# Kernel tuning notes

Measured on AMD Instinct MI355X. Metric: run time of the kernel, lower is better.

Reference implementation:

```python
import jax, jax.numpy as jnp
import numpy as np

B, N, F, R, DEG, STEPS = 4, 1024, 128, 16, 16, 2


def setup_inputs() -> dict:
    key = jax.random.key(0)
    ks = jax.random.split(key, 12)
    BN = B * N
    E = BN * DEG

    def edges(k):
        # edges kept within each graph of size N, then offset per graph
        e = jax.random.randint(k, (2, E), 0, N)
        off = jnp.repeat(jnp.arange(B, dtype=jnp.int32) * N, N * DEG)
        return e + off[None, :]

    return {
        "x_s": jax.random.normal(ks[0], (BN, F), jnp.float32),
        "edge_index_s": edges(ks[1]),
        "x_t": jax.random.normal(ks[2], (BN, F), jnp.float32),
        "edge_index_t": edges(ks[3]),
        "W1_self": jax.random.normal(ks[4], (F, F), jnp.float32) / np.float32(np.sqrt(F)),
        "W1_nbr": jax.random.normal(ks[5], (F, F), jnp.float32) / np.float32(np.sqrt(F)),
        "b1": jnp.zeros((F,), jnp.float32),
        "W2_self": jax.random.normal(ks[6], (R, R), jnp.float32) / np.float32(np.sqrt(R)),
        "W2_nbr": jax.random.normal(ks[7], (R, R), jnp.float32) / np.float32(np.sqrt(R)),
        "b2": jnp.zeros((R,), jnp.float32),
        "Wm1": jax.random.normal(ks[8], (R, R), jnp.float32) / np.float32(np.sqrt(R)),
        "bm1": jnp.zeros((R,), jnp.float32),
        "Wm2": jax.random.normal(ks[9], (R, 1), jnp.float32) / np.float32(np.sqrt(R)),
        "bm2": jnp.zeros((1,), jnp.float32),
        "r_steps": jax.random.normal(ks[10], (STEPS, B, N, R), jnp.float32),
    }


def _psi(x, ei, Ws, Wn, b):
    # simple GraphConv: self transform + summed neighbor transform
    agg = jax.ops.segment_sum(x[ei[0]], ei[1], num_segments=x.shape[0])
    return jax.nn.relu(x @ Ws + agg @ Wn + b)


def reference(x_s, edge_index_s, x_t, edge_index_t, W1_self, W1_nbr, b1,
              W2_self, W2_nbr, b2, Wm1, bm1, Wm2, bm2, r_steps):
    # psi_1 on both graphs, then dense-batch to [B, N, F] (equal-size graphs,
    # so masks are all-True and masked_softmax == softmax)
    h_s = _psi(x_s, edge_index_s, W1_self, W1_nbr, b1).reshape(B, N, F)
    h_t = _psi(x_t, edge_index_t, W1_self, W1_nbr, b1).reshape(B, N, F)

    S_hat = jnp.einsum('bsf,btf->bst', h_s, h_t)  # [B, Ns, Nt]
    S_0 = jax.nn.softmax(S_hat, axis=-1)

    for i in range(STEPS):
        S = jax.nn.softmax(S_hat, axis=-1)
        r_s = r_steps[i]                             # [B, N, R]
        r_t = jnp.einsum('bst,bsr->btr', S, r_s)     # S^T @ r_s
        o_s = _psi(r_s.reshape(B * N, R), edge_index_s, W2_self, W2_nbr, b2).reshape(B, N, R)
        o_t = _psi(r_t.reshape(B * N, R), edge_index_t, W2_self, W2_nbr, b2).reshape(B, N, R)
        D = o_s[:, :, None, :] - o_t[:, None, :, :]  # [B, Ns, Nt, R]
        upd = (jax.nn.relu(D @ Wm1 + bm1) @ Wm2 + bm2)[..., 0]
        S_hat = S_hat + upd

    S_L = jax.nn.softmax(S_hat, axis=-1)
    return (S_0, S_L)
```

## Files before the change

kernel.cpp:

```cpp
#include <hip/hip_runtime.h>

#define B_ 4
#define N_ 1024
#define F_ 128
#define R_ 16
#define E_ 65536
#define BN_ 4096

__global__ __launch_bounds__(256) void hist_k(
    const int* __restrict__ eis, const int* __restrict__ eit, int* __restrict__ counts) {
  const int* ei = blockIdx.y ? eit : eis;
  int* c = counts + blockIdx.y * BN_;
  int e = blockIdx.x * 256 + threadIdx.x;
  atomicAdd(c + ei[E_ + e], 1);
}

__global__ __launch_bounds__(256) void csr_scan(
    const int* __restrict__ counts, int* __restrict__ offs, int* __restrict__ cursor) {
  const int* c = counts + blockIdx.x * BN_;
  int* o = offs + blockIdx.x * (BN_ + 1);
  int* cur = cursor + blockIdx.x * BN_;
  int tid = threadIdx.x;
  int base = tid * 16;
  int local[16], sum = 0;
#pragma unroll
  for (int i = 0; i < 16; i++) { local[i] = sum; sum += c[base + i]; }
  __shared__ int csum[256];
  csum[tid] = sum;
  __syncthreads();
  for (int d = 1; d < 256; d <<= 1) {
    int v = (tid >= d) ? csum[tid - d] : 0;
    __syncthreads();
    csum[tid] += v;
    __syncthreads();
  }
  int prev = (tid == 0) ? 0 : csum[tid - 1];
#pragma unroll
  for (int i = 0; i < 16; i++) { int off = prev + local[i]; o[base + i] = off; cur[base + i] = off; }
  if (tid == 255) o[BN_] = csum[255];
}

__global__ __launch_bounds__(256) void csr_fill(
    const int* __restrict__ eis, const int* __restrict__ eit,
    int* __restrict__ cursor, int* __restrict__ csr) {
  const int* ei = blockIdx.y ? eit : eis;
  int* cur = cursor + blockIdx.y * BN_;
  int* cs = csr + blockIdx.y * E_;
  int e = blockIdx.x * 256 + threadIdx.x;
  int src = ei[e], dst = ei[E_ + e];
  int pos = atomicAdd(cur + dst, 1);
  cs[pos] = src;
}

__global__ __launch_bounds__(256) void gather_f(
    const float* __restrict__ xs, const float* __restrict__ xt,
    const int* __restrict__ csr, const int* __restrict__ offs,
    float* __restrict__ aggs, float* __restrict__ aggt) {
  const float* x = blockIdx.y ? xt : xs;
  const int* cs = csr + blockIdx.y * E_;
  const int* of = offs + blockIdx.y * (BN_ + 1);
  float* agg = blockIdx.y ? aggt : aggs;
  int node = blockIdx.x * 8 + (threadIdx.x >> 5);
  int ch4 = (threadIdx.x & 31) * 4;
  int j0 = of[node], j1 = of[node + 1];
  float4 a0 = {0, 0, 0, 0}, a1 = {0, 0, 0, 0}, a2 = {0, 0, 0, 0}, a3 = {0, 0, 0, 0};
  int j = j0;
  for (; j + 3 < j1; j += 4) {
    int s0 = cs[j], s1 = cs[j + 1], s2 = cs[j + 2], s3 = cs[j + 3];
    float4 v0 = *(const float4*)(x + (size_t)s0 * F_ + ch4);
    float4 v1 = *(const float4*)(x + (size_t)s1 * F_ + ch4);
    float4 v2 = *(const float4*)(x + (size_t)s2 * F_ + ch4);
    float4 v3 = *(const float4*)(x + (size_t)s3 * F_ + ch4);
    a0.x += v0.x; a0.y += v0.y; a0.z += v0.z; a0.w += v0.w;
    a1.x += v1.x; a1.y += v1.y; a1.z += v1.z; a1.w += v1.w;
    a2.x += v2.x; a2.y += v2.y; a2.z += v2.z; a2.w += v2.w;
    a3.x += v3.x; a3.y += v3.y; a3.z += v3.z; a3.w += v3.w;
  }
  for (; j < j1; j++) {
    float4 v = *(const float4*)(x + (size_t)cs[j] * F_ + ch4);
    a0.x += v.x; a0.y += v.y; a0.z += v.z; a0.w += v.w;
  }
  float4 o;
  o.x = (a0.x + a1.x) + (a2.x + a3.x);
  o.y = (a0.y + a1.y) + (a2.y + a3.y);
  o.z = (a0.z + a1.z) + (a2.z + a3.z);
  o.w = (a0.w + a1.w) + (a2.w + a3.w);
  *(float4*)(agg + (size_t)node * F_ + ch4) = o;
}

__global__ __launch_bounds__(256) void psi1_gemm(
    const float* __restrict__ xs, const float* __restrict__ aggs,
    const float* __restrict__ xt, const float* __restrict__ aggt,
    const float* __restrict__ Ws, const float* __restrict__ Wn,
    const float* __restrict__ bias, float* __restrict__ hs, float* __restrict__ ht) {
  const float* x   = blockIdx.z ? xt   : xs;
  const float* agg = blockIdx.z ? aggt : aggs;
  float*       h   = blockIdx.z ? ht   : hs;
  int n0 = blockIdx.x * 64, m0 = blockIdx.y * 64;
  int tid = threadIdx.x, tx = tid & 15, ty = tid >> 4;
  __shared__ __align__(16) float sA[16][68];
  __shared__ __align__(16) float sB[16][68];
  float acc[4][4] = {};
  for (int phase = 0; phase < 2; phase++) {
    const float* A  = phase ? agg : x;
    const float* Bw = phase ? Wn  : Ws;
    for (int kb = 0; kb < F_; kb += 16) {
      int row = tid >> 2, k4 = (tid & 3) * 4;
      float4 va = *(const float4*)(A + (size_t)(m0 + row) * F_ + kb + k4);
      sA[k4 + 0][row] = va.x; sA[k4 + 1][row] = va.y;
      sA[k4 + 2][row] = va.z; sA[k4 + 3][row] = va.w;
      int k = tid >> 4, n4 = (tid & 15) * 4;
      *(float4*)&sB[k][n4] = *(const float4*)(Bw + (size_t)(kb + k) * F_ + n0 + n4);
      __syncthreads();
#pragma unroll
      for (int kk = 0; kk < 16; kk++) {
        float a[4], bb[4];
        *(float4*)a  = *(const float4*)&sA[kk][ty * 4];
        *(float4*)bb = *(const float4*)&sB[kk][tx * 4];
#pragma unroll
        for (int i = 0; i < 4; i++)
#pragma unroll
          for (int j = 0; j < 4; j++) acc[i][j] += a[i] * bb[j];
      }
      __syncthreads();
    }
  }
  float4 bv = *(const float4*)(bias + n0 + tx * 4);
  float bj[4] = {bv.x, bv.y, bv.z, bv.w};
#pragma unroll
  for (int i = 0; i < 4; i++) {
    int m = m0 + ty * 4 + i;
    float4 o;
    o.x = fmaxf(acc[i][0] + bj[0], 0.f); o.y = fmaxf(acc[i][1] + bj[1], 0.f);
    o.z = fmaxf(acc[i][2] + bj[2], 0.f); o.w = fmaxf(acc[i][3] + bj[3], 0.f);
    *(float4*)(h + (size_t)m * F_ + n0 + tx * 4) = o;
  }
}

__global__ __launch_bounds__(256) void shat_gemm(
    const float* __restrict__ hs, const float* __restrict__ ht, float* __restrict__ S) {
  int b = blockIdx.z;
  int n0 = blockIdx.x * 128, m0 = blockIdx.y * 128;
  int tid = threadIdx.x, tx = tid & 15, ty = tid >> 4;
  __shared__ __align__(16) float sA[16][132];
  __shared__ __align__(16) float sB[16][132];
  float acc[8][8] = {};
  const float* Ag = hs + (size_t)(b * N_ + m0) * F_;
  const float* Bg = ht + (size_t)(b * N_ + n0) * F_;
  for (int kb = 0; kb < F_; kb += 16) {
#pragma unroll
    for (int l = 0; l < 2; l++) {
      int idx = tid + l * 256;
      int row = idx >> 2, k4 = (idx & 3) * 4;
      float4 va = *(const float4*)(Ag + (size_t)row * F_ + kb + k4);
      sA[k4 + 0][row] = va.x; sA[k4 + 1][row] = va.y;
      sA[k4 + 2][row] = va.z; sA[k4 + 3][row] = va.w;
      float4 vb = *(const float4*)(Bg + (size_t)row * F_ + kb + k4);
      sB[k4 + 0][row] = vb.x; sB[k4 + 1][row] = vb.y;
      sB[k4 + 2][row] = vb.z; sB[k4 + 3][row] = vb.w;
    }
    __syncthreads();
#pragma unroll
    for (int kk = 0; kk < 16; kk++) {
      float a[8], bb[8];
      *(float4*)&a[0]  = *(const float4*)&sA[kk][ty * 8];
      *(float4*)&a[4]  = *(const float4*)&sA[kk][ty * 8 + 4];
      *(float4*)&bb[0] = *(const float4*)&sB[kk][tx * 8];
      *(float4*)&bb[4] = *(const float4*)&sB[kk][tx * 8 + 4];
#pragma unroll
      for (int i = 0; i < 8; i++)
#pragma unroll
        for (int j = 0; j < 8; j++) acc[i][j] += a[i] * bb[j];
    }
    __syncthreads();
  }
#pragma unroll
  for (int i = 0; i < 8; i++) {
    size_t off = ((size_t)(b * N_ + m0 + ty * 8 + i)) * N_ + n0 + tx * 8;
    float4 o0 = {acc[i][0], acc[i][1], acc[i][2], acc[i][3]};
    float4 o1 = {acc[i][4], acc[i][5], acc[i][6], acc[i][7]};
    *(float4*)(S + off) = o0; *(float4*)(S + off + 4) = o1;
  }
}

__global__ __launch_bounds__(256) void row_stats(
    const float* __restrict__ in, float2* __restrict__ stats) {
  int row = blockIdx.x;
  float4 v = ((const float4*)(in + (size_t)row * N_))[threadIdx.x];
  float m = fmaxf(fmaxf(v.x, v.y), fmaxf(v.z, v.w));
#pragma unroll
  for (int o = 32; o > 0; o >>= 1) m = fmaxf(m, __shfl_down(m, o, 64));
  __shared__ float rmax[4], rsum[4];
  int wave = threadIdx.x >> 6, lane = threadIdx.x & 63;
  if (lane == 0) rmax[wave] = m;
  __syncthreads();
  m = fmaxf(fmaxf(rmax[0], rmax[1]), fmaxf(rmax[2], rmax[3]));
  float s = __expf(v.x - m) + __expf(v.y - m) + __expf(v.z - m) + __expf(v.w - m);
#pragma unroll
  for (int o = 32; o > 0; o >>= 1) s += __shfl_down(s, o, 64);
  if (lane == 0) rsum[wave] = s;
  __syncthreads();
  if (threadIdx.x == 0) {
    float tot = rsum[0] + rsum[1] + rsum[2] + rsum[3];
    stats[row] = make_float2(m, 1.f / tot);
  }
}

template <bool WRITE_S>
__global__ __launch_bounds__(256) void rt_part_k(
    const float* __restrict__ S, const float2* __restrict__ stats,
    const float* __restrict__ rs, float* __restrict__ part, float* __restrict__ Sout) {
  int b = blockIdx.z, c = blockIdx.y, t0 = blockIdx.x * 256;
  int tid = threadIdx.x;
  int s0 = c * 32;
  __shared__ float rsh[32][16];
  __shared__ float sstat[64];
  if (tid < 128) {
    int srow = tid >> 2, c4 = (tid & 3) * 4;
    float4 v = *(const float4*)(rs + ((size_t)(b * N_ + s0 + srow)) * R_ + c4);
    rsh[srow][c4] = v.x; rsh[srow][c4 + 1] = v.y;
    rsh[srow][c4 + 2] = v.z; rsh[srow][c4 + 3] = v.w;
  } else if (tid < 192) {
    sstat[tid - 128] = ((const float*)(stats + b * N_ + s0))[tid - 128];
  }
  __syncthreads();
  float acc[16] = {};
  const size_t base = ((size_t)(b * N_ + s0)) * N_ + t0 + tid;
  const float* Sp = S + base;
  float* So = WRITE_S ? (Sout + base) : nullptr;
#pragma unroll
  for (int s = 0; s < 32; s++) {
    float p = __expf(Sp[(size_t)s * N_] - sstat[2 * s]) * sstat[2 * s + 1];
    if (WRITE_S) So[(size_t)s * N_] = p;
#pragma unroll
    for (int r = 0; r < 16; r++) acc[r] += p * rsh[s][r];
  }
  float* o = part + ((size_t)((b * 32 + c) * N_) + t0 + tid) * R_;
  *(float4*)(o + 0)  = *(float4*)&acc[0];
  *(float4*)(o + 4)  = *(float4*)&acc[4];
  *(float4*)(o + 8)  = *(float4*)&acc[8];
  *(float4*)(o + 12) = *(float4*)&acc[12];
}

__global__ __launch_bounds__(256) void rt_reduce(
    const float* __restrict__ part, float* __restrict__ rt) {
  int gid = blockIdx.x * 256 + threadIdx.x;
  int b = gid >> 12, tr = gid & 4095;
  const float* p = part + (size_t)b * (32 * N_ * R_) + (size_t)tr * 4;
  float4 acc = {0.f, 0.f, 0.f, 0.f};
#pragma unroll
  for (int c = 0; c < 32; c++) {
    float4 v = *(const float4*)(p + (size_t)c * (N_ * R_));
    acc.x += v.x; acc.y += v.y; acc.z += v.z; acc.w += v.w;
  }
  ((float4*)rt)[gid] = acc;
}

__global__ __launch_bounds__(256) void gpsi2p(
    const float* __restrict__ vs, const float* __restrict__ vt,
    const int* __restrict__ csr, const int* __restrict__ offs,
    const float* __restrict__ W2s, const float* __restrict__ W2n,
    const float* __restrict__ b2, const float* __restrict__ Wm1,
    float* __restrict__ Ps, float* __restrict__ Pt4) {
  const float* v = blockIdx.y ? vt : vs;
  const int* cs = csr + blockIdx.y * E_;
  const int* of = offs + blockIdx.y * (BN_ + 1);
  int col = threadIdx.x & 15, row = threadIdx.x >> 4;
  int node = blockIdx.x * 16 + row;
  int j0 = of[node], j1 = of[node + 1];
  float a0 = 0.f, a1 = 0.f, a2 = 0.f, a3 = 0.f;
  int j = j0;
  for (; j + 3 < j1; j += 4) {
    int s0 = cs[j], s1 = cs[j + 1], s2 = cs[j + 2], s3 = cs[j + 3];
    a0 += v[(size_t)s0 * R_ + col];
    a1 += v[(size_t)s1 * R_ + col];
    a2 += v[(size_t)s2 * R_ + col];
    a3 += v[(size_t)s3 * R_ + col];
  }
  for (; j < j1; j++) a0 += v[(size_t)cs[j] * R_ + col];
  __shared__ float sWs[16][16], sWn[16][16], sWm[16][17];
  __shared__ float sv[16][17], sa[16][17], so[16][17];
  sWs[row][col] = W2s[row * 16 + col];
  sWn[row][col] = W2n[row * 16 + col];
  sWm[row][col] = Wm1[row * 16 + col];
  sv[row][col] = v[(size_t)node * R_ + col];
  sa[row][col] = (a0 + a1) + (a2 + a3);
  __syncthreads();
  float o = b2[col];
#pragma unroll
  for (int k = 0; k < 16; k++) o += sv[row][k] * sWs[k][col] + sa[row][k] * sWn[k][col];
  so[row][col] = fmaxf(o, 0.f);
  __syncthreads();
  float p = 0;
#pragma unroll
  for (int k = 0; k < 16; k++) p += so[row][k] * sWm[k][col];
  if (blockIdx.y) {
    Pt4[((size_t)(col >> 2) * BN_ + node) * 4 + (col & 3)] = p;
  } else {
    Ps[(size_t)node * R_ + col] = p;
  }
}

template <int LAST>
__global__ __launch_bounds__(256) void upd_row4(
    float* __restrict__ Shat, const float* __restrict__ Ps, const float* __restrict__ Pt4,
    const float* __restrict__ bm1, const float* __restrict__ Wm2,
    const float* __restrict__ bm2, float2* __restrict__ stats, float* __restrict__ SL) {
  int b = blockIdx.y, s0 = blockIdx.x * 2;
  int tid = threadIdx.x;
  __shared__ float sc[2][16], sw16[16];
  __shared__ float wred[2][4];
  if (tid < 32) sc[tid >> 4][tid & 15] =
      Ps[((size_t)(b * N_ + s0 + (tid >> 4))) * R_ + (tid & 15)] + bm1[tid & 15];
  if (tid < 16) sw16[tid] = Wm2[tid];
  float bm2v = bm2[0];
  __syncthreads();
  float vals[2][4];
#pragma unroll
  for (int tile = 0; tile < 4; tile++) {
    int gt = b * N_ + tile * 256 + tid;
    float pt[16];
    *(float4*)&pt[0]  = *(const float4*)(Pt4 + ((size_t)0 * BN_ + gt) * 4);
    *(float4*)&pt[4]  = *(const float4*)(Pt4 + ((size_t)1 * BN_ + gt) * 4);
    *(float4*)&pt[8]  = *(const float4*)(Pt4 + ((size_t)2 * BN_ + gt) * 4);
    *(float4*)&pt[12] = *(const float4*)(Pt4 + ((size_t)3 * BN_ + gt) * 4);
#pragma unroll
    for (int rr = 0; rr < 2; rr++) {
      size_t off = ((size_t)(b * N_ + s0 + rr)) * N_ + tile * 256 + tid;
      float sum = bm2v;
#pragma unroll
      for (int r = 0; r < 16; r++) sum += fmaxf(sc[rr][r] - pt[r], 0.f) * sw16[r];
      float vv = Shat[off] + sum;
      vals[rr][tile] = vv;
      if (!LAST) Shat[off] = vv;
    }
  }
  int wave = tid >> 6, lane = tid & 63;
#pragma unroll
  for (int rr = 0; rr < 2; rr++) {
    float m = fmaxf(fmaxf(vals[rr][0], vals[rr][1]), fmaxf(vals[rr][2], vals[rr][3]));
#pragma unroll
    for (int o = 32; o > 0; o >>= 1) m = fmaxf(m, __shfl_down(m, o, 64));
    if (lane == 0) wred[rr][wave] = m;
  }
  __syncthreads();
  float M[2];
#pragma unroll
  for (int rr = 0; rr < 2; rr++)
    M[rr] = fmaxf(fmaxf(wred[rr][0], wred[rr][1]), fmaxf(wred[rr][2], wred[rr][3]));
  __syncthreads();
  float e[2][4];
#pragma unroll
  for (int rr = 0; rr < 2; rr++) {
    e[rr][0] = __expf(vals[rr][0] - M[rr]); e[rr][1] = __expf(vals[rr][1] - M[rr]);
    e[rr][2] = __expf(vals[rr][2] - M[rr]); e[rr][3] = __expf(vals[rr][3] - M[rr]);
    float l = (e[rr][0] + e[rr][1]) + (e[rr][2] + e[rr][3]);
#pragma unroll
    for (int o = 32; o > 0; o >>= 1) l += __shfl_down(l, o, 64);
    if (lane == 0) wred[rr][wave] = l;
  }
  __syncthreads();
#pragma unroll
  for (int rr = 0; rr < 2; rr++) {
    float l = (wred[rr][0] + wred[rr][1]) + (wred[rr][2] + wred[rr][3]);
    size_t rowoff = ((size_t)(b * N_ + s0 + rr)) * N_;
    if (LAST) {
      float inv = 1.f / l;
      SL[rowoff + 0 * 256 + tid] = e[rr][0] * inv;
      SL[rowoff + 1 * 256 + tid] = e[rr][1] * inv;
      SL[rowoff + 2 * 256 + tid] = e[rr][2] * inv;
      SL[rowoff + 3 * 256 + tid] = e[rr][3] * inv;
    } else {
      if (tid == 0) stats[b * N_ + s0 + rr] = make_float2(M[rr], 1.f / l);
    }
  }
}

extern "C" void kernel_launch(void* const* d_in, const int* in_sizes, int n_in,
                              void* d_out, int out_size, void* d_ws, size_t ws_size,
                              hipStream_t stream) {
  const float* x_s = (const float*)d_in[0];
  const int*   ei_s = (const int*)d_in[1];
  const float* x_t = (const float*)d_in[2];
  const int*   ei_t = (const int*)d_in[3];
  const float* W1s = (const float*)d_in[4];
  const float* W1n = (const float*)d_in[5];
  const float* b1  = (const float*)d_in[6];
  const float* W2s = (const float*)d_in[7];
  const float* W2n = (const float*)d_in[8];
  const float* b2  = (const float*)d_in[9];
  const float* Wm1 = (const float*)d_in[10];
  const float* bm1 = (const float*)d_in[11];
  const float* Wm2 = (const float*)d_in[12];
  const float* bm2 = (const float*)d_in[13];
  const float* r_steps = (const float*)d_in[14];

  float* out = (float*)d_out;
  float* S0 = out;
  float* SL = out + (size_t)B_ * N_ * N_;

  float* ws = (float*)d_ws;
  float* agg_s = ws;
  float* agg_t = ws + 524288;
  float* h_s   = ws + 1048576;
  float* h_t   = ws + 1572864;
  float* part  = ws;
  float* Shat  = ws + 2097152;
  float* rtb   = ws + 6291456;
  float2* stats = (float2*)(ws + 6356992);
  float* Ps    = ws + 6488064;
  float* Pt4   = ws + 6553600;
  int* counts  = (int*)(ws + 6619136);
  int* cursor  = (int*)(ws + 6627328);
  int* offs    = (int*)(ws + 6635520);
  int* csr     = (int*)(ws + 6643720);

  hipMemsetAsync(counts, 0, 2 * BN_ * sizeof(int), stream);
  hist_k<<<dim3(E_ / 256, 2), 256, 0, stream>>>(ei_s, ei_t, counts);
  csr_scan<<<2, 256, 0, stream>>>(counts, offs, cursor);
  csr_fill<<<dim3(E_ / 256, 2), 256, 0, stream>>>(ei_s, ei_t, cursor, csr);

  gather_f<<<dim3(BN_ / 8, 2), 256, 0, stream>>>(x_s, x_t, csr, offs, agg_s, agg_t);
  psi1_gemm<<<dim3(2, 64, 2), 256, 0, stream>>>(x_s, agg_s, x_t, agg_t, W1s, W1n, b1, h_s, h_t);

  shat_gemm<<<dim3(8, 8, 4), 256, 0, stream>>>(h_s, h_t, Shat);
  row_stats<<<B_ * N_, 256, 0, stream>>>(Shat, stats);

  const float* rs0 = r_steps;
  rt_part_k<true><<<dim3(4, 32, 4), 256, 0, stream>>>(Shat, stats, rs0, part, S0);
  rt_reduce<<<64, 256, 0, stream>>>(part, rtb);
  gpsi2p<<<dim3(256, 2), 256, 0, stream>>>(rs0, rtb, csr, offs, W2s, W2n, b2, Wm1, Ps, Pt4);
  upd_row4<0><<<dim3(N_ / 2, B_), 256, 0, stream>>>(Shat, Ps, Pt4, bm1, Wm2, bm2, stats, nullptr);

  const float* rs1 = r_steps + (size_t)B_ * N_ * R_;
  rt_part_k<false><<<dim3(4, 32, 4), 256, 0, stream>>>(Shat, stats, rs1, part, nullptr);
  rt_reduce<<<64, 256, 0, stream>>>(part, rtb);
  gpsi2p<<<dim3(256, 2), 256, 0, stream>>>(rs1, rtb, csr, offs, W2s, W2n, b2, Wm1, Ps, Pt4);
  upd_row4<1><<<dim3(N_ / 2, B_), 256, 0, stream>>>(Shat, Ps, Pt4, bm1, Wm2, bm2, nullptr, SL);
}
```

Baseline: 243.3 us.

## Fuse softmax row stats into S_hat GEMM and use padded adjacency lists

The separate row_stats pass over S_hat is replaced by per-tile max/sum-exp partials computed in the GEMM epilogue. These are merged inside the first rt_part_k launch. The three-kernel CSR build (histogram, scan, fill) becomes a single atomic fill into fixed-capacity per-node lists of 48 slots. This removes a full read of the large S_hat matrix and several launches, but it assumes no node exceeds 48 incoming edges and needs more workspace.

```diff
diff --git a/kernel.cpp b/kernel.cpp
--- a/kernel.cpp
+++ b/kernel.cpp
@@ -6,67 +6,36 @@
 #define R_ 16
 #define E_ 65536
 #define BN_ 4096
-
-__global__ __launch_bounds__(256) void hist_k(
-    const int* __restrict__ eis, const int* __restrict__ eit, int* __restrict__ counts) {
+#define CAP_ 48
+
+__global__ __launch_bounds__(256) void csr_fill_direct(
+    const int* __restrict__ eis, const int* __restrict__ eit,
+    int* __restrict__ counts, int* __restrict__ csr) {
   const int* ei = blockIdx.y ? eit : eis;
-  int* c = counts + blockIdx.y * BN_;
-  int e = blockIdx.x * 256 + threadIdx.x;
-  atomicAdd(c + ei[E_ + e], 1);
-}
-
-__global__ __launch_bounds__(256) void csr_scan(
-    const int* __restrict__ counts, int* __restrict__ offs, int* __restrict__ cursor) {
-  const int* c = counts + blockIdx.x * BN_;
-  int* o = offs + blockIdx.x * (BN_ + 1);
-  int* cur = cursor + blockIdx.x * BN_;
-  int tid = threadIdx.x;
-  int base = tid * 16;
-  int local[16], sum = 0;
-#pragma unroll
-  for (int i = 0; i < 16; i++) { local[i] = sum; sum += c[base + i]; }
-  __shared__ int csum[256];
-  csum[tid] = sum;
-  __syncthreads();
-  for (int d = 1; d < 256; d <<= 1) {
-    int v = (tid >= d) ? csum[tid - d] : 0;
-    __syncthreads();
-    csum[tid] += v;
-    __syncthreads();
-  }
-  int prev = (tid == 0) ? 0 : csum[tid - 1];
-#pragma unroll
-  for (int i = 0; i < 16; i++) { int off = prev + local[i]; o[base + i] = off; cur[base + i] = off; }
-  if (tid == 255) o[BN_] = csum[255];
-}
-
-__global__ __launch_bounds__(256) void csr_fill(
-    const int* __restrict__ eis, const int* __restrict__ eit,
-    int* __restrict__ cursor, int* __restrict__ csr) {
-  const int* ei = blockIdx.y ? eit : eis;
-  int* cur = cursor + blockIdx.y * BN_;
-  int* cs = csr + blockIdx.y * E_;
+  int* cnt = counts + blockIdx.y * BN_;
+  int* cs = csr + blockIdx.y * (BN_ * CAP_);
   int e = blockIdx.x * 256 + threadIdx.x;
   int src = ei[e], dst = ei[E_ + e];
-  int pos = atomicAdd(cur + dst, 1);
-  cs[pos] = src;
+  int pos = atomicAdd(cnt + dst, 1);
+  cs[dst * CAP_ + pos] = src;
 }
 
 __global__ __launch_bounds__(256) void gather_f(
     const float* __restrict__ xs, const float* __restrict__ xt,
-    const int* __restrict__ csr, const int* __restrict__ offs,
+    const int* __restrict__ csr, const int* __restrict__ counts,
     float* __restrict__ aggs, float* __restrict__ aggt) {
   const float* x = blockIdx.y ? xt : xs;
-  const int* cs = csr + blockIdx.y * E_;
-  const int* of = offs + blockIdx.y * (BN_ + 1);
+  const int* cs = csr + (size_t)blockIdx.y * (BN_ * CAP_);
+  const int* cnt = counts + blockIdx.y * BN_;
   float* agg = blockIdx.y ? aggt : aggs;
   int node = blockIdx.x * 8 + (threadIdx.x >> 5);
   int ch4 = (threadIdx.x & 31) * 4;
-  int j0 = of[node], j1 = of[node + 1];
+  const int* lst = cs + node * CAP_;
+  int j1 = cnt[node];
   float4 a0 = {0, 0, 0, 0}, a1 = {0, 0, 0, 0}, a2 = {0, 0, 0, 0}, a3 = {0, 0, 0, 0};
-  int j = j0;
+  int j = 0;
   for (; j + 3 < j1; j += 4) {
-    int s0 = cs[j], s1 = cs[j + 1], s2 = cs[j + 2], s3 = cs[j + 3];
+    int s0 = lst[j], s1 = lst[j + 1], s2 = lst[j + 2], s3 = lst[j + 3];
     float4 v0 = *(const float4*)(x + (size_t)s0 * F_ + ch4);
     float4 v1 = *(const float4*)(x + (size_t)s1 * F_ + ch4);
     float4 v2 = *(const float4*)(x + (size_t)s2 * F_ + ch4);
@@ -77,7 +46,7 @@
     a3.x += v3.x; a3.y += v3.y; a3.z += v3.z; a3.w += v3.w;
   }
   for (; j < j1; j++) {
-    float4 v = *(const float4*)(x + (size_t)cs[j] * F_ + ch4);
+    float4 v = *(const float4*)(x + (size_t)lst[j] * F_ + ch4);
     a0.x += v.x; a0.y += v.y; a0.z += v.z; a0.w += v.w;
   }
   float4 o;
@@ -138,7 +107,8 @@
 }
 
 __global__ __launch_bounds__(256) void shat_gemm(
-    const float* __restrict__ hs, const float* __restrict__ ht, float* __restrict__ S) {
+    const float* __restrict__ hs, const float* __restrict__ ht,
+    float* __restrict__ S, float2* __restrict__ pstats) {
   int b = blockIdx.z;
   int n0 = blockIdx.x * 128, m0 = blockIdx.y * 128;
   int tid = threadIdx.x, tx = tid & 15, ty = tid >> 4;
@@ -181,34 +151,28 @@
     float4 o1 = {acc[i][4], acc[i][5], acc[i][6], acc[i][7]};
     *(float4*)(S + off) = o0; *(float4*)(S + off + 4) = o1;
   }
-}
-
-__global__ __launch_bounds__(256) void row_stats(
-    const float* __restrict__ in, float2* __restrict__ stats) {
-  int row = blockIdx.x;
-  float4 v = ((const float4*)(in + (size_t)row * N_))[threadIdx.x];
-  float m = fmaxf(fmaxf(v.x, v.y), fmaxf(v.z, v.w));
-#pragma unroll
-  for (int o = 32; o > 0; o >>= 1) m = fmaxf(m, __shfl_down(m, o, 64));
-  __shared__ float rmax[4], rsum[4];
-  int wave = threadIdx.x >> 6, lane = threadIdx.x & 63;
-  if (lane == 0) rmax[wave] = m;
-  __syncthreads();
-  m = fmaxf(fmaxf(rmax[0], rmax[1]), fmaxf(rmax[2], rmax[3]));
-  float s = __expf(v.x - m) + __expf(v.y - m) + __expf(v.z - m) + __expf(v.w - m);
-#pragma unroll
-  for (int o = 32; o > 0; o >>= 1) s += __shfl_down(s, o, 64);
-  if (lane == 0) rsum[wave] = s;
-  __syncthreads();
-  if (threadIdx.x == 0) {
-    float tot = rsum[0] + rsum[1] + rsum[2] + rsum[3];
-    stats[row] = make_float2(m, 1.f / tot);
-  }
-}
-
-template <bool WRITE_S>
+#pragma unroll
+  for (int i = 0; i < 8; i++) {
+    float m = acc[i][0];
+#pragma unroll
+    for (int j = 1; j < 8; j++) m = fmaxf(m, acc[i][j]);
+#pragma unroll
+    for (int o = 8; o > 0; o >>= 1) m = fmaxf(m, __shfl_down(m, o, 16));
+    m = __shfl(m, 0, 16);
+    float l = 0.f;
+#pragma unroll
+    for (int j = 0; j < 8; j++) l += __expf(acc[i][j] - m);
+#pragma unroll
+    for (int o = 8; o > 0; o >>= 1) l += __shfl_down(l, o, 16);
+    if (tx == 0)
+      pstats[((size_t)(b * 8 + blockIdx.x)) * N_ + m0 + ty * 8 + i] = make_float2(m, l);
+  }
+}
+
+template <bool FIRST>
 __global__ __launch_bounds__(256) void rt_part_k(
     const float* __restrict__ S, const float2* __restrict__ stats,
+    const float2* __restrict__ pstats,
     const float* __restrict__ rs, float* __restrict__ part, float* __restrict__ Sout) {
   int b = blockIdx.z, c = blockIdx.y, t0 = blockIdx.x * 256;
   int tid = threadIdx.x;
@@ -220,18 +184,31 @@
     float4 v = *(const float4*)(rs + ((size_t)(b * N_ + s0 + srow)) * R_ + c4);
     rsh[srow][c4] = v.x; rsh[srow][c4 + 1] = v.y;
     rsh[srow][c4 + 2] = v.z; rsh[srow][c4 + 3] = v.w;
-  } else if (tid < 192) {
+  } else if (FIRST && tid < 160) {
+    int s = tid - 128;
+    float2 v[8];
+    float m = -3.4e38f;
+#pragma unroll
+    for (int t = 0; t < 8; t++) {
+      v[t] = pstats[((size_t)(b * 8 + t)) * N_ + s0 + s];
+      m = fmaxf(m, v[t].x);
+    }
+    float L = 0.f;
+#pragma unroll
+    for (int t = 0; t < 8; t++) L += __expf(v[t].x - m) * v[t].y;
+    sstat[2 * s] = m; sstat[2 * s + 1] = 1.f / L;
+  } else if (!FIRST && tid >= 128 && tid < 192) {
     sstat[tid - 128] = ((const float*)(stats + b * N_ + s0))[tid - 128];
   }
   __syncthreads();
   float acc[16] = {};
   const size_t base = ((size_t)(b * N_ + s0)) * N_ + t0 + tid;
   const float* Sp = S + base;
-  float* So = WRITE_S ? (Sout + base) : nullptr;
+  float* So = FIRST ? (Sout + base) : nullptr;
 #pragma unroll
   for (int s = 0; s < 32; s++) {
     float p = __expf(Sp[(size_t)s * N_] - sstat[2 * s]) * sstat[2 * s + 1];
-    if (WRITE_S) So[(size_t)s * N_] = p;
+    if (FIRST) So[(size_t)s * N_] = p;
 #pragma unroll
     for (int r = 0; r < 16; r++) acc[r] += p * rsh[s][r];
   }
@@ -258,26 +235,27 @@
 
 __global__ __launch_bounds__(256) void gpsi2p(
     const float* __restrict__ vs, const float* __restrict__ vt,
-    const int* __restrict__ csr, const int* __restrict__ offs,
+    const int* __restrict__ csr, const int* __restrict__ counts,
     const float* __restrict__ W2s, const float* __restrict__ W2n,
     const float* __restrict__ b2, const float* __restrict__ Wm1,
     float* __restrict__ Ps, float* __restrict__ Pt4) {
   const float* v = blockIdx.y ? vt : vs;
-  const int* cs = csr + blockIdx.y * E_;
-  const int* of = offs + blockIdx.y * (BN_ + 1);
+  const int* cs = csr + (size_t)blockIdx.y * (BN_ * CAP_);
+  const int* cnt = counts + blockIdx.y * BN_;
   int col = threadIdx.x & 15, row = threadIdx.x >> 4;
   int node = blockIdx.x * 16 + row;
-  int j0 = of[node], j1 = of[node + 1];
+  const int* lst = cs + node * CAP_;
+  int j1 = cnt[node];
   float a0 = 0.f, a1 = 0.f, a2 = 0.f, a3 = 0.f;
-  int j = j0;
+  int j = 0;
   for (; j + 3 < j1; j += 4) {
-    int s0 = cs[j], s1 = cs[j + 1], s2 = cs[j + 2], s3 = cs[j + 3];
+    int s0 = lst[j], s1 = lst[j + 1], s2 = lst[j + 2], s3 = lst[j + 3];
     a0 += v[(size_t)s0 * R_ + col];
     a1 += v[(size_t)s1 * R_ + col];
     a2 += v[(size_t)s2 * R_ + col];
     a3 += v[(size_t)s3 * R_ + col];
   }
-  for (; j < j1; j++) a0 += v[(size_t)cs[j] * R_ + col];
+  for (; j < j1; j++) a0 += v[(size_t)lst[j] * R_ + col];
   __shared__ float sWs[16][16], sWn[16][16], sWm[16][17];
   __shared__ float sv[16][17], sa[16][17], so[16][17];
   sWs[row][col] = W2s[row * 16 + col];
@@ -408,33 +386,29 @@
   float* Shat  = ws + 2097152;
   float* rtb   = ws + 6291456;
   float2* stats = (float2*)(ws + 6356992);
+  float2* pstats = (float2*)(ws + 6365184);
   float* Ps    = ws + 6488064;
   float* Pt4   = ws + 6553600;
   int* counts  = (int*)(ws + 6619136);
-  int* cursor  = (int*)(ws + 6627328);
-  int* offs    = (int*)(ws + 6635520);
-  int* csr     = (int*)(ws + 6643720);
+  int* csr     = (int*)(ws + 6627328);
 
   hipMemsetAsync(counts, 0, 2 * BN_ * sizeof(int), stream);
-  hist_k<<<dim3(E_ / 256, 2), 256, 0, stream>>>(ei_s, ei_t, counts);
-  csr_scan<<<2, 256, 0, stream>>>(counts, offs, cursor);
-  csr_fill<<<dim3(E_ / 256, 2), 256, 0, stream>>>(ei_s, ei_t, cursor, csr);
-
-  gather_f<<<dim3(BN_ / 8, 2), 256, 0, stream>>>(x_s, x_t, csr, offs, agg_s, agg_t);
+  csr_fill_direct<<<dim3(E_ / 256, 2), 256, 0, stream>>>(ei_s, ei_t, counts, csr);
+
+  gather_f<<<dim3(BN_ / 8, 2), 256, 0, stream>>>(x_s, x_t, csr, counts, agg_s, agg_t);
   psi1_gemm<<<dim3(2, 64, 2), 256, 0, stream>>>(x_s, agg_s, x_t, agg_t, W1s, W1n, b1, h_s, h_t);
 
-  shat_gemm<<<dim3(8, 8, 4), 256, 0, stream>>>(h_s, h_t, Shat);
-  row_stats<<<B_ * N_, 256, 0, stream>>>(Shat, stats);
+  shat_gemm<<<dim3(8, 8, 4), 256, 0, stream>>>(h_s, h_t, Shat, pstats);
 
   const float* rs0 = r_steps;
-  rt_part_k<true><<<dim3(4, 32, 4), 256, 0, stream>>>(Shat, stats, rs0, part, S0);
+  rt_part_k<true><<<dim3(4, 32, 4), 256, 0, stream>>>(Shat, nullptr, pstats, rs0, part, S0);
   rt_reduce<<<64, 256, 0, stream>>>(part, rtb);
-  gpsi2p<<<dim3(256, 2), 256, 0, stream>>>(rs0, rtb, csr, offs, W2s, W2n, b2, Wm1, Ps, Pt4);
+  gpsi2p<<<dim3(256, 2), 256, 0, stream>>>(rs0, rtb, csr, counts, W2s, W2n, b2, Wm1, Ps, Pt4);
   upd_row4<0><<<dim3(N_ / 2, B_), 256, 0, stream>>>(Shat, Ps, Pt4, bm1, Wm2, bm2, stats, nullptr);
 
   const float* rs1 = r_steps + (size_t)B_ * N_ * R_;
-  rt_part_k<false><<<dim3(4, 32, 4), 256, 0, stream>>>(Shat, stats, rs1, part, nullptr);
+  rt_part_k<false><<<dim3(4, 32, 4), 256, 0, stream>>>(Shat, stats, nullptr, rs1, part, nullptr);
   rt_reduce<<<64, 256, 0, stream>>>(part, rtb);
-  gpsi2p<<<dim3(256, 2), 256, 0, stream>>>(rs1, rtb, csr, offs, W2s, W2n, b2, Wm1, Ps, Pt4);
+  gpsi2p<<<dim3(256, 2), 256, 0, stream>>>(rs1, rtb, csr, counts, W2s, W2n, b2, Wm1, Ps, Pt4);
   upd_row4<1><<<dim3(N_ / 2, B_), 256, 0, stream>>>(Shat, Ps, Pt4, bm1, Wm2, bm2, nullptr, SL);
 }
```

Result: faster. 232.7 us (-4.4%).
